# Kernel tuning notes

Measured on AMD Instinct MI355X. Metric: run time of the kernel, lower is better.

Reference implementation:

```python
import jax, jax.numpy as jnp
import numpy as np

N_HEADS = 8

def setup_inputs() -> dict:
    key = jax.random.key(0)
    ks = jax.random.split(key, 12)
    B, S2, C, H, W = 2, 2048, 1280, 256, 256
    s = 0.02  # weight init scale
    return {
        'hidden_states': jax.random.normal(ks[0], (B, S2, C), dtype=jnp.float32),
        'src_mask': (jax.random.uniform(ks[1], (B, 1, H, W)) > 0.5).astype(jnp.float32),
        'attn_wq': jax.random.normal(ks[2], (C, C), dtype=jnp.float32) * s,
        'attn_wk': jax.random.normal(ks[3], (C, C), dtype=jnp.float32) * s,
        'attn_wv': jax.random.normal(ks[4], (C, C), dtype=jnp.float32) * s,
        'out_w': jax.random.normal(ks[5], (C, C), dtype=jnp.float32) * s,
        'out_b': jnp.zeros((C,), dtype=jnp.float32),
        'proc_wq': jax.random.normal(ks[6], (C, C), dtype=jnp.float32) * s,
        'proc_wk': jax.random.normal(ks[7], (C, C), dtype=jnp.float32) * s,
        'proc_wv': jax.random.normal(ks[8], (C, C), dtype=jnp.float32) * s,
        'ww': jax.random.normal(ks[9], (C + 1, 1), dtype=jnp.float32) * s,
        'wb': jnp.zeros((1,), dtype=jnp.float32),
    }


def reference(hidden_states, src_mask, attn_wq, attn_wk, attn_wv, out_w, out_b,
              proc_wq, proc_wk, proc_wv, ww, wb):
    B, S2, C = hidden_states.shape
    S = S2 // 2  # condition_flag=False: sequence is two images concatenated
    _, _, H, W = src_mask.shape
    r = int(np.sqrt((H * W) / S))  # nearest-neighbor downsample ratio
    # F.interpolate(mode='nearest') with exact integer ratio == strided slice
    m = src_mask[:, 0, ::r, ::r].reshape(B, S, 1)          # [B, S, 1]
    mask = jnp.concatenate([m, m], axis=1)                 # [B, 2S, 1]
    # sigmoid gate blending the two query projections
    gate_in = jnp.concatenate([hidden_states, mask], axis=-1)  # [B, 2S, C+1]
    w = jax.nn.sigmoid(gate_in @ ww + wb)                  # [B, 2S, 1]
    query = (hidden_states @ attn_wq) * w + (hidden_states @ proc_wq) * (1.0 - w)
    # keys/values: first half through attn's projections, second half through processor's
    e1, e2 = hidden_states[:, :S], hidden_states[:, S:]
    key = jnp.concatenate([e1 @ attn_wk, e2 @ proc_wk], axis=1)
    value = jnp.concatenate([e1 @ attn_wv, e2 @ proc_wv], axis=1)
    d = C // N_HEADS
    def split_heads(x):
        return x.reshape(B, S2, N_HEADS, d).transpose(0, 2, 1, 3)  # [B, H, S2, d]
    qh, kh, vh = split_heads(query), split_heads(key), split_heads(value)
    scale = float(1.0 / np.sqrt(d))
    scores = jnp.einsum('bhqd,bhkd->bhqk', qh, kh) * scale
    probs = jax.nn.softmax(scores, axis=-1)
    out = jnp.einsum('bhqk,bhkd->bhqd', probs, vh)
    out = out.transpose(0, 2, 1, 3).reshape(B, S2, C)
    out = out @ out_w + out_b
    # residual connection, rescale_output_factor == 1
    return out + hidden_states
```

## Files before the change

kernel.cpp:

```cpp
#include <hip/hip_runtime.h>

typedef unsigned short u16;
typedef u16 u16x4 __attribute__((ext_vector_type(4)));
typedef u16 u16x8 __attribute__((ext_vector_type(8)));
typedef __bf16 bf16x8 __attribute__((ext_vector_type(8)));
typedef float f32x4 __attribute__((ext_vector_type(4)));
typedef unsigned u32x4 __attribute__((ext_vector_type(4)));

#define DEVI __device__ __forceinline__

#if __has_builtin(__builtin_amdgcn_exp2f)
#define EXP2F __builtin_amdgcn_exp2f
#else
#define EXP2F exp2f
#endif

DEVI u16 f2b(float f) {
  unsigned u = __builtin_bit_cast(unsigned, f);
  u += 0x7fffu + ((u >> 16) & 1u);
  return (u16)(u >> 16);
}

DEVI float b2f(u16 v) { return __builtin_bit_cast(float, (unsigned)v << 16); }

DEVI unsigned cvtpk_bf16(float lo, float hi) {
  unsigned r;
  asm("v_cvt_pk_bf16_f32 %0, %1, %2" : "=v"(r) : "v"(lo), "v"(hi));
  return r;
}

DEVI f32x4 mfma16(u16x8 a, u16x8 b, f32x4 c) {
  return __builtin_amdgcn_mfma_f32_16x16x32_bf16(
      __builtin_bit_cast(bf16x8, a), __builtin_bit_cast(bf16x8, b), c, 0, 0, 0);
}

DEVI void async_copy16(const u16* g, u16* l) {
  __builtin_amdgcn_global_load_lds(
      (__attribute__((address_space(1))) unsigned int*)(g),
      (__attribute__((address_space(3))) unsigned int*)(l), 16, 0, 0);
}

DEVI void fence_barrier() {
  asm volatile("" ::: "memory");
  __builtin_amdgcn_s_barrier();
  asm volatile("" ::: "memory");
}

__global__ void prep_kernel(const float* __restrict__ hs, const float* __restrict__ mask,
                            const float* __restrict__ ww, const float* __restrict__ wb,
                            u16* __restrict__ hsb, float* __restrict__ wgate) {
  int token = blockIdx.x;
  int tid = threadIdx.x;
  const float* row = hs + (size_t)token * 1280;
  u16* orow = hsb + (size_t)token * 1280;
  float acc = 0.f;
#pragma unroll
  for (int i = 0; i < 5; i++) {
    int c = i * 256 + tid;
    float v = row[c];
    orow[c] = f2b(v);
    acc += v * ww[c];
  }
#pragma unroll
  for (int off = 1; off < 64; off <<= 1) acc += __shfl_xor(acc, off);
  __shared__ float partial[4];
  int wid = tid >> 6;
  if ((tid & 63) == 0) partial[wid] = acc;
  __syncthreads();
  if (tid == 0) {
    float tot = partial[0] + partial[1] + partial[2] + partial[3];
    int b = token >> 11, t = token & 2047;
    int s = t & 1023;
    float mv = mask[b * 65536 + ((s >> 5) * 8) * 256 + (s & 31) * 8];
    float z = tot + mv * ww[1280] + wb[0];
    wgate[token] = 1.f / (1.f + __expf(-z));
  }
}

__global__ void wtrans_kernel(const float* w0, const float* w1, const float* w2,
                              const float* w3, const float* w4, const float* w5,
                              const float* w6, u16* __restrict__ out) {
  const float* src;
  switch (blockIdx.z) {
    case 0: src = w0; break; case 1: src = w1; break; case 2: src = w2; break;
    case 3: src = w3; break; case 4: src = w4; break; case 5: src = w5; break;
    default: src = w6; break;
  }
  u16* dst = out + (size_t)blockIdx.z * 1280 * 1280;
  __shared__ float tile[32][33];
  int tx = threadIdx.x & 31, ty = threadIdx.x >> 5;
  int k0 = blockIdx.x * 32, n0 = blockIdx.y * 32;
#pragma unroll
  for (int r = 0; r < 4; r++)
    tile[ty + r * 8][tx] = src[(size_t)(k0 + ty + r * 8) * 1280 + n0 + tx];
  __syncthreads();
#pragma unroll
  for (int r = 0; r < 4; r++)
    dst[(size_t)(n0 + ty + r * 8) * 1280 + k0 + tx] = f2b(tile[tx][ty + r * 8]);
}

__launch_bounds__(256)
__global__ void gemm_qkv_kernel(const u16* __restrict__ A, const u16* __restrict__ Wt,
                                u16* __restrict__ Qa, u16* __restrict__ Qp,
                                u16* __restrict__ Kout, u16* __restrict__ VTout) {
  const int K = 1280, N = 1280;
  const size_t WSZ = (size_t)1280 * 1280;
  __shared__ u16 As[128 * 32];
  __shared__ u16 Bs[128 * 32];

  int tid = threadIdx.x;
  int wid = tid >> 6, lane = tid & 63;
  int nb = blockIdx.x, mb = blockIdx.y, z = blockIdx.z;
  int m0 = mb * 128, n0 = nb * 128;
  bool first = ((m0 & 2047) < 1024);

  const u16* B;
  switch (z) {
    case 0:  B = Wt + 0 * WSZ; break;
    case 1:  B = Wt + 4 * WSZ; break;
    case 2:  B = first ? Wt + 1 * WSZ : Wt + 5 * WSZ; break;
    default: B = first ? Wt + 2 * WSZ : Wt + 6 * WSZ; break;
  }

  f32x4 zero = {0.f, 0.f, 0.f, 0.f};
  f32x4 acc[4][4];
#pragma unroll
  for (int i = 0; i < 4; i++)
#pragma unroll
    for (int j = 0; j < 4; j++) acc[i][j] = zero;

  int wr = wid >> 1, wc = wid & 1;

  for (int kk = 0; kk < 40; kk++) {
    int k0 = kk * 32;
#pragma unroll
    for (int i = 0; i < 2; i++) {
      int slot = i * 256 + tid;
      int row = slot >> 2, seg = slot & 3;
      async_copy16(A + (size_t)(m0 + row) * K + k0 + seg * 8, As + (size_t)(i * 256 + wid * 64) * 8);
      async_copy16(B + (size_t)(n0 + row) * K + k0 + seg * 8, Bs + (size_t)(i * 256 + wid * 64) * 8);
    }
    asm volatile("s_waitcnt vmcnt(0)" ::: "memory");
    __syncthreads();

    u16x8 af[4], bfr[4];
#pragma unroll
    for (int mi = 0; mi < 4; mi++)
      af[mi] = *(const u16x8*)(As + (wr * 64 + mi * 16 + (lane & 15)) * 32 + (lane >> 4) * 8);
#pragma unroll
    for (int ni = 0; ni < 4; ni++)
      bfr[ni] = *(const u16x8*)(Bs + (wc * 64 + ni * 16 + (lane & 15)) * 32 + (lane >> 4) * 8);
#pragma unroll
    for (int mi = 0; mi < 4; mi++)
#pragma unroll
      for (int ni = 0; ni < 4; ni++)
        acc[mi][ni] = mfma16(af[mi], bfr[ni], acc[mi][ni]);
    __syncthreads();
  }

  if (z == 3) {
#pragma unroll
    for (int mi = 0; mi < 4; mi++)
#pragma unroll
      for (int ni = 0; ni < 4; ni++) {
        int row0 = m0 + wr * 64 + mi * 16 + ((lane >> 4) << 2);
        int col = n0 + wc * 64 + ni * 16 + (lane & 15);
        int b = row0 >> 11, s = row0 & 2047;
        int h = col / 160, c_in = col - h * 160;
        u16x4 v = {f2b(acc[mi][ni][0]), f2b(acc[mi][ni][1]),
                   f2b(acc[mi][ni][2]), f2b(acc[mi][ni][3])};
        *(u16x4*)(VTout + ((size_t)(b * 8 + h) * 160 + c_in) * 2048 + s) = v;
      }
  } else {
    u16* Cb = (z == 0) ? Qa : (z == 1) ? Qp : Kout;
#pragma unroll
    for (int mi = 0; mi < 4; mi++)
#pragma unroll
      for (int ni = 0; ni < 4; ni++)
#pragma unroll
        for (int r = 0; r < 4; r++) {
          int row = m0 + wr * 64 + mi * 16 + ((lane >> 4) << 2) + r;
          int col = n0 + wc * 64 + ni * 16 + (lane & 15);
          Cb[(size_t)row * N + col] = f2b(acc[mi][ni][r]);
        }
  }
}

__global__ void qblend_kernel(u16* __restrict__ Qa, const u16* __restrict__ Qp,
                              const float* __restrict__ wgate, float qscale) {
  int idx = blockIdx.x * 256 + threadIdx.x;
  int token = idx / 160;
  float w = wgate[token];
  u16x8 qa = *(const u16x8*)(Qa + (size_t)idx * 8);
  u16x8 qp = *(const u16x8*)(Qp + (size_t)idx * 8);
  u16x8 o;
#pragma unroll
  for (int j = 0; j < 8; j++)
    o[j] = f2b((w * b2f(qa[j]) + (1.f - w) * b2f(qp[j])) * qscale);
  *(u16x8*)(Qa + (size_t)idx * 8) = o;
}

template <int SPLIT>
__launch_bounds__(256)
__global__ void flash_kernel(const u16* __restrict__ Q, const u16* __restrict__ Kg,
                             const u16* __restrict__ VTg, u16* __restrict__ O,
                             u16* __restrict__ Opart, float* __restrict__ MLbuf) {
  const int C = 1280;
  int bid = blockIdx.x;
  int qb = bid & 31, h = (bid >> 5) & 7, b = bid >> 8;
  int sp = (SPLIT > 1) ? (int)blockIdx.y : 0;
  int tid = threadIdx.x, wid = tid >> 6, lane = tid & 63;

  int t0, NT;
  if (SPLIT == 3) { t0 = sp * 11; NT = (sp < 2) ? 11 : 10; }
  else if (SPLIT == 1) { t0 = 0; NT = 32; }
  else { t0 = sp * (32 / SPLIT); NT = 32 / SPLIT; }

  const size_t baseQ = ((size_t)(b * 2048 + qb * 64)) * C + h * 160;
  const size_t baseK = ((size_t)(b * 2048)) * C + h * 160;
  const size_t baseVT = (size_t)(b * 8 + h) * 160 * 2048;

  __shared__ u16 Ks[64 * 168];
  __shared__ u16 Vts[160 * 64];

  const u16* kbase = Kg + baseK + (size_t)(t0 * 64) * C;
  const u16* vbase = VTg + baseVT + t0 * 64;
  unsigned koff[6];
#pragma unroll
  for (int j = 0; j < 6; j++) {
    int i = wid + 4 * j;
    if (i > 20) i = wid + 16;
    int gc = i * 64 + lane;
    int r = gc / 21, ch = gc - r * 21;
    int chs = ch < 20 ? ch : 19;
    koff[j] = (unsigned)(r * C + chs * 8);
  }
  unsigned voff[5];
#pragma unroll
  for (int j = 0; j < 5; j++) {
    int i = wid + 4 * j;
    int gc = i * 64 + lane;
    int c = gc >> 3, jj = gc & 7;
    voff[j] = (unsigned)(c * 2048 + ((jj ^ (c & 7)) << 3));
  }

#define STAGE_K()                                       \
  do {                                                  \
    _Pragma("unroll") for (int j = 0; j < 6; j++) {     \
      int i = wid + 4 * j;                              \
      if (i > 20) i = wid + 16;                         \
      async_copy16(kbase + koff[j], Ks + i * 512);      \
    }                                                   \
  } while (0)
#define STAGE_V()                                               \
  do {                                                          \
    _Pragma("unroll") for (int j = 0; j < 5; j++)               \
        async_copy16(vbase + voff[j], Vts + (wid + 4 * j) * 512); \
  } while (0)

  const int addr0 = ((lane & 15) + 16 * (((lane >> 4) * 2 + 0) & 3)) << 2;
  const int addr1 = ((lane & 15) + 16 * (((lane >> 4) * 2 + 1) & 3)) << 2;
  const bool hihalf = (lane >= 32);

  u16x8 qf[5];
  {
    int row = wid * 16 + (lane & 15);
    const u16* qrow = Q + baseQ + (size_t)row * C;
#pragma unroll
    for (int ks = 0; ks < 5; ks++)
      qf[ks] = *(const u16x8*)(qrow + ks * 32 + (lane >> 4) * 8);
  }

  f32x4 zero = {0.f, 0.f, 0.f, 0.f};
  f32x4 oacc[10];
#pragma unroll
  for (int i = 0; i < 10; i++) oacc[i] = zero;
  float mrow = -1e30f, lrow = 0.f;

  STAGE_K();
  STAGE_V();

  for (int kti = 0; kti < NT; kti++) {
    bool last = (kti == NT - 1);
    asm volatile("s_waitcnt vmcnt(5)" ::: "memory");
    fence_barrier();

    f32x4 sc[4];
#pragma unroll
    for (int ct = 0; ct < 4; ct++) {
      f32x4 a = zero;
#pragma unroll
      for (int ks = 0; ks < 5; ks++) {
        u16x8 kf = *(const u16x8*)(&Ks[(ct * 16 + (lane & 15)) * 168 + ks * 32 + (lane >> 4) * 8]);
        a = mfma16(kf, qf[ks], a);
      }
      sc[ct] = a;
    }

    fence_barrier();
    if (!last) { kbase += 64 * C; STAGE_K(); }

    float m = sc[0][0];
#pragma unroll
    for (int ct = 0; ct < 4; ct++)
#pragma unroll
      for (int r = 0; r < 4; r++) m = fmaxf(m, sc[ct][r]);
    m = fmaxf(m, __shfl_xor(m, 16));
    m = fmaxf(m, __shfl_xor(m, 32));

    if (__any(m > mrow + 8.f)) {
      float mnew = fmaxf(mrow, m);
      float alpha = EXP2F(mrow - mnew);
      mrow = mnew;
      float rs = 0.f;
#pragma unroll
      for (int ct = 0; ct < 4; ct++)
#pragma unroll
        for (int r = 0; r < 4; r++) {
          float p = EXP2F(sc[ct][r] - mnew);
          sc[ct][r] = p;
          rs += p;
        }
      lrow = lrow * alpha + rs;
#pragma unroll
      for (int ci = 0; ci < 10; ci++) oacc[ci] *= alpha;
    } else {
      float rs = 0.f;
#pragma unroll
      for (int ct = 0; ct < 4; ct++)
#pragma unroll
        for (int r = 0; r < 4; r++) {
          float p = EXP2F(sc[ct][r] - mrow);
          sc[ct][r] = p;
          rs += p;
        }
      lrow += rs;
    }

    unsigned pk0[4], pk1[4];
#pragma unroll
    for (int ct = 0; ct < 4; ct++) {
      pk0[ct] = cvtpk_bf16(sc[ct][0], sc[ct][1]);
      pk1[ct] = cvtpk_bf16(sc[ct][2], sc[ct][3]);
    }

    if (!last) { asm volatile("s_waitcnt vmcnt(6)" ::: "memory"); }
    else       { asm volatile("s_waitcnt vmcnt(0)" ::: "memory"); }
    fence_barrier();

#pragma unroll
    for (int kt2 = 0; kt2 < 2; kt2++) {
      const int cA = kt2 * 2, cB = kt2 * 2 + 1;
      int a0 = __builtin_amdgcn_ds_bpermute(addr0, (int)pk0[cA]);
      int a1 = __builtin_amdgcn_ds_bpermute(addr0, (int)pk1[cA]);
      int a2 = __builtin_amdgcn_ds_bpermute(addr1, (int)pk0[cA]);
      int a3 = __builtin_amdgcn_ds_bpermute(addr1, (int)pk1[cA]);
      int b0 = __builtin_amdgcn_ds_bpermute(addr0, (int)pk0[cB]);
      int b1 = __builtin_amdgcn_ds_bpermute(addr0, (int)pk1[cB]);
      int b2 = __builtin_amdgcn_ds_bpermute(addr1, (int)pk0[cB]);
      int b3 = __builtin_amdgcn_ds_bpermute(addr1, (int)pk1[cB]);
      u32x4 d;
      d[0] = (unsigned)(hihalf ? b0 : a0);
      d[1] = (unsigned)(hihalf ? b1 : a1);
      d[2] = (unsigned)(hihalf ? b2 : a2);
      d[3] = (unsigned)(hihalf ? b3 : a3);
      u16x8 pf = __builtin_bit_cast(u16x8, d);
#pragma unroll
      for (int ci = 0; ci < 10; ci++) {
        int c = ci * 16 + (lane & 15);
        int jl = kt2 * 4 + (lane >> 4);
        u16x8 vf = *(const u16x8*)(&Vts[c * 64 + ((jl ^ (c & 7)) << 3)]);
        oacc[ci] = mfma16(vf, pf, oacc[ci]);
      }
    }

    fence_barrier();
    if (!last) { vbase += 64; STAGE_V(); }
  }
#undef STAGE_K
#undef STAGE_V

  lrow += __shfl_xor(lrow, 16);
  lrow += __shfl_xor(lrow, 32);
  float linv = 1.f / lrow;

  int qrow = qb * 64 + wid * 16 + (lane & 15);
  if constexpr (SPLIT > 1) {
    size_t g0 = (size_t)sp * 4096 + (size_t)b * 2048 + qrow;
#pragma unroll
    for (int ci = 0; ci < 10; ci++) {
      int col = h * 160 + ci * 16 + ((lane >> 4) << 2);
      u16x4 v = {f2b(oacc[ci][0] * linv), f2b(oacc[ci][1] * linv),
                 f2b(oacc[ci][2] * linv), f2b(oacc[ci][3] * linv)};
      *(u16x4*)(Opart + g0 * 1280 + col) = v;
    }
    if (lane < 16) {
      size_t mi = (g0 * 8 + h) * 2;
      MLbuf[mi] = mrow;
      MLbuf[mi + 1] = lrow;
    }
  } else {
#pragma unroll
    for (int ci = 0; ci < 10; ci++) {
      int col = h * 160 + ci * 16 + ((lane >> 4) << 2);
      u16x4 v = {f2b(oacc[ci][0] * linv), f2b(oacc[ci][1] * linv),
                 f2b(oacc[ci][2] * linv), f2b(oacc[ci][3] * linv)};
      *(u16x4*)(O + ((size_t)(b * 2048) + qrow) * C + col) = v;
    }
  }
}

__global__ void combine_kernel(const u16* __restrict__ Opart, const float* __restrict__ MLbuf,
                               u16* __restrict__ O) {
  int idx = blockIdx.x * 256 + threadIdx.x;
  int token = idx / 160;
  int h = (idx - token * 160) / 20;
  size_t i0 = ((size_t)token * 8 + h) * 2;
  const size_t MLP = (size_t)4096 * 16;
  float m0 = MLbuf[i0], l0 = MLbuf[i0 + 1];
  float m1 = MLbuf[i0 + MLP], l1 = MLbuf[i0 + MLP + 1];
  float m2 = MLbuf[i0 + 2 * MLP], l2 = MLbuf[i0 + 2 * MLP + 1];
  float m = fmaxf(fmaxf(m0, m1), m2);
  float w0 = EXP2F(m0 - m) * l0, w1 = EXP2F(m1 - m) * l1, w2 = EXP2F(m2 - m) * l2;
  float inv = 1.f / (w0 + w1 + w2);
  w0 *= inv; w1 *= inv; w2 *= inv;
  const size_t OPP = (size_t)655360;
  u16x8 a = *(const u16x8*)(Opart + (size_t)idx * 8);
  u16x8 c = *(const u16x8*)(Opart + (OPP + idx) * 8);
  u16x8 d = *(const u16x8*)(Opart + (2 * OPP + idx) * 8);
  u16x8 o;
#pragma unroll
  for (int j = 0; j < 8; j++)
    o[j] = f2b(b2f(a[j]) * w0 + b2f(c[j]) * w1 + b2f(d[j]) * w2);
  *(u16x8*)(O + (size_t)idx * 8) = o;
}

__launch_bounds__(256)
__global__ void gemm_out_kernel(const u16* __restrict__ A, const u16* __restrict__ Bt,
                                float* __restrict__ Cf, const float* __restrict__ bias,
                                const float* __restrict__ resid) {
  const int K = 1280, N = 1280;
  __shared__ u16 As[128 * 32];
  __shared__ u16 Bs[128 * 32];

  int tid = threadIdx.x;
  int wid = tid >> 6, lane = tid & 63;
  int nb = blockIdx.x, mb = blockIdx.y;
  int m0 = mb * 128, n0 = nb * 128;

  f32x4 zero = {0.f, 0.f, 0.f, 0.f};
  f32x4 acc[4][4];
#pragma unroll
  for (int i = 0; i < 4; i++)
#pragma unroll
    for (int j = 0; j < 4; j++) acc[i][j] = zero;

  int wr = wid >> 1, wc = wid & 1;

  for (int kk = 0; kk < 40; kk++) {
    int k0 = kk * 32;
#pragma unroll
    for (int i = 0; i < 2; i++) {
      int slot = i * 256 + tid;
      int row = slot >> 2, seg = slot & 3;
      async_copy16(A + (size_t)(m0 + row) * K + k0 + seg * 8, As + (size_t)(i * 256 + wid * 64) * 8);
      async_copy16(Bt + (size_t)(n0 + row) * K + k0 + seg * 8, Bs + (size_t)(i * 256 + wid * 64) * 8);
    }
    asm volatile("s_waitcnt vmcnt(0)" ::: "memory");
    __syncthreads();

    u16x8 af[4], bfr[4];
#pragma unroll
    for (int mi = 0; mi < 4; mi++)
      af[mi] = *(const u16x8*)(As + (wr * 64 + mi * 16 + (lane & 15)) * 32 + (lane >> 4) * 8);
#pragma unroll
    for (int ni = 0; ni < 4; ni++)
      bfr[ni] = *(const u16x8*)(Bs + (wc * 64 + ni * 16 + (lane & 15)) * 32 + (lane >> 4) * 8);
#pragma unroll
    for (int mi = 0; mi < 4; mi++)
#pragma unroll
      for (int ni = 0; ni < 4; ni++)
        acc[mi][ni] = mfma16(af[mi], bfr[ni], acc[mi][ni]);
    __syncthreads();
  }

#pragma unroll
  for (int mi = 0; mi < 4; mi++)
#pragma unroll
    for (int ni = 0; ni < 4; ni++)
#pragma unroll
      for (int r = 0; r < 4; r++) {
        int row = m0 + wr * 64 + mi * 16 + ((lane >> 4) << 2) + r;
        int col = n0 + wc * 64 + ni * 16 + (lane & 15);
        Cf[(size_t)row * N + col] = acc[mi][ni][r] + bias[col] + resid[(size_t)row * N + col];
      }
}

extern "C" void kernel_launch(void* const* d_in, const int* in_sizes, int n_in,
                              void* d_out, int out_size, void* d_ws, size_t ws_size,
                              hipStream_t stream) {
  const float* hs      = (const float*)d_in[0];
  const float* mask    = (const float*)d_in[1];
  const float* attn_wq = (const float*)d_in[2];
  const float* attn_wk = (const float*)d_in[3];
  const float* attn_wv = (const float*)d_in[4];
  const float* out_w   = (const float*)d_in[5];
  const float* out_b   = (const float*)d_in[6];
  const float* proc_wq = (const float*)d_in[7];
  const float* proc_wk = (const float*)d_in[8];
  const float* proc_wv = (const float*)d_in[9];
  const float* ww      = (const float*)d_in[10];
  const float* wb      = (const float*)d_in[11];
  float* out = (float*)d_out;

  char* ws = (char*)d_ws;
  const size_t TOK = (size_t)4096 * 1280;
  u16* hsb = (u16*)(ws);
  u16* Qb  = (u16*)(ws + 2 * TOK);
  u16* Kb  = (u16*)(ws + 4 * TOK);
  u16* VTb = (u16*)(ws + 6 * TOK);
  u16* AOb = (u16*)(ws + 8 * TOK);
  u16* Wt  = (u16*)(ws + 10 * TOK);
  float* wgate = (float*)(ws + 10 * TOK + (size_t)7 * 1280 * 1280 * 2);
  char* extra = ws + 10 * TOK + (size_t)7 * 1280 * 1280 * 2 + 16384;
  u16* Opart = (u16*)extra;
  float* MLbuf = (float*)(extra + (size_t)3 * 4096 * 1280 * 2);
  size_t need = (size_t)(extra - ws) + (size_t)3 * 4096 * 1280 * 2 + (size_t)3 * 4096 * 8 * 8;

  prep_kernel<<<4096, 256, 0, stream>>>(hs, mask, ww, wb, hsb, wgate);
  wtrans_kernel<<<dim3(40, 40, 7), 256, 0, stream>>>(attn_wq, attn_wk, attn_wv, out_w,
                                                     proc_wq, proc_wk, proc_wv, Wt);
  const size_t WSZ = (size_t)1280 * 1280;
  gemm_qkv_kernel<<<dim3(10, 32, 4), 256, 0, stream>>>(hsb, Wt, Qb, AOb, Kb, VTb);
  const float qscale = 0.11405505533858971f;
  qblend_kernel<<<2560, 256, 0, stream>>>(Qb, AOb, wgate, qscale);

  if (ws_size >= need) {
    flash_kernel<3><<<dim3(512, 3), 256, 0, stream>>>(Qb, Kb, VTb, nullptr, Opart, MLbuf);
    combine_kernel<<<2560, 256, 0, stream>>>(Opart, MLbuf, AOb);
  } else {
    flash_kernel<1><<<dim3(512, 1), 256, 0, stream>>>(Qb, Kb, VTb, AOb, nullptr, nullptr);
  }
  gemm_out_kernel<<<dim3(10, 32), 256, 0, stream>>>(AOb, Wt + 3 * WSZ, out, out_b, hs);
}
```

Measured before the change: 240.4 us.

## Fuse query gate blend into QKV GEMM epilogue and swizzle flash K tile

The QKV GEMM now computes both query projections in the same block for z<2, with each block taking 64 output columns from each weight. The sigmoid-gated blend and scale are applied in the epilogue, which removes the separate qblend kernel and its extra read/write pass over two query buffers. Separately, the flash kernel's K shared tile drops its 168-element padded rows in favour of an XOR swizzle. That cuts async copies per tile from 6 to 5 and shrinks LDS use. Inner loop shapes change for the dual case, which may affect register pressure and scheduling.

```diff
diff --git a/kernel.cpp b/kernel.cpp
--- a/kernel.cpp
+++ b/kernel.cpp
@@ -101,26 +101,27 @@
 
 __launch_bounds__(256)
 __global__ void gemm_qkv_kernel(const u16* __restrict__ A, const u16* __restrict__ Wt,
-                                u16* __restrict__ Qa, u16* __restrict__ Qp,
-                                u16* __restrict__ Kout, u16* __restrict__ VTout) {
+                                const float* __restrict__ wgate, float qscale,
+                                u16* __restrict__ Qout, u16* __restrict__ Kout,
+                                u16* __restrict__ VTout) {
   const int K = 1280, N = 1280;
   const size_t WSZ = (size_t)1280 * 1280;
   __shared__ u16 As[128 * 32];
-  __shared__ u16 Bs[128 * 32];
+  __shared__ u16 Bs[64 * 32];
+  __shared__ u16 Bs2[64 * 32];
 
   int tid = threadIdx.x;
   int wid = tid >> 6, lane = tid & 63;
+  int q = lane & 15, jl = lane >> 4;
   int nb = blockIdx.x, mb = blockIdx.y, z = blockIdx.z;
   int m0 = mb * 128, n0 = nb * 128;
+  bool dual = (z < 2);
   bool first = ((m0 & 2047) < 1024);
 
-  const u16* B;
-  switch (z) {
-    case 0:  B = Wt + 0 * WSZ; break;
-    case 1:  B = Wt + 4 * WSZ; break;
-    case 2:  B = first ? Wt + 1 * WSZ : Wt + 5 * WSZ; break;
-    default: B = first ? Wt + 2 * WSZ : Wt + 6 * WSZ; break;
-  }
+  const u16 *B0, *B1;
+  if (dual)        { B0 = Wt + 0 * WSZ; B1 = Wt + 4 * WSZ; }
+  else if (z == 2) { B0 = first ? Wt + 1 * WSZ : Wt + 5 * WSZ; B1 = B0; }
+  else             { B0 = first ? Wt + 2 * WSZ : Wt + 6 * WSZ; B1 = B0; }
 
   f32x4 zero = {0.f, 0.f, 0.f, 0.f};
   f32x4 acc[4][4];
@@ -130,6 +131,7 @@
     for (int j = 0; j < 4; j++) acc[i][j] = zero;
 
   int wr = wid >> 1, wc = wid & 1;
+  int brow = tid >> 2, bseg = tid & 3;
 
   for (int kk = 0; kk < 40; kk++) {
     int k0 = kk * 32;
@@ -138,66 +140,87 @@
       int slot = i * 256 + tid;
       int row = slot >> 2, seg = slot & 3;
       async_copy16(A + (size_t)(m0 + row) * K + k0 + seg * 8, As + (size_t)(i * 256 + wid * 64) * 8);
-      async_copy16(B + (size_t)(n0 + row) * K + k0 + seg * 8, Bs + (size_t)(i * 256 + wid * 64) * 8);
+    }
+    if (dual) {
+      int nrow = n0 + (z << 6) + brow;
+      async_copy16(B0 + (size_t)nrow * K + k0 + bseg * 8, Bs + (size_t)tid * 8);
+      async_copy16(B1 + (size_t)nrow * K + k0 + bseg * 8, Bs2 + (size_t)tid * 8);
+    } else {
+      async_copy16(B0 + (size_t)(n0 + brow) * K + k0 + bseg * 8, Bs + (size_t)tid * 8);
+      async_copy16(B0 + (size_t)(n0 + 64 + brow) * K + k0 + bseg * 8, Bs2 + (size_t)tid * 8);
     }
     asm volatile("s_waitcnt vmcnt(0)" ::: "memory");
     __syncthreads();
 
-    u16x8 af[4], bfr[4];
+    u16x8 af[4];
 #pragma unroll
     for (int mi = 0; mi < 4; mi++)
-      af[mi] = *(const u16x8*)(As + (wr * 64 + mi * 16 + (lane & 15)) * 32 + (lane >> 4) * 8);
-#pragma unroll
-    for (int ni = 0; ni < 4; ni++)
-      bfr[ni] = *(const u16x8*)(Bs + (wc * 64 + ni * 16 + (lane & 15)) * 32 + (lane >> 4) * 8);
+      af[mi] = *(const u16x8*)(As + (wr * 64 + mi * 16 + q) * 32 + jl * 8);
+    if (dual) {
+#pragma unroll
+      for (int ni = 0; ni < 2; ni++) {
+        u16x8 bf0 = *(const u16x8*)(Bs + (wc * 32 + ni * 16 + q) * 32 + jl * 8);
+        u16x8 bf1 = *(const u16x8*)(Bs2 + (wc * 32 + ni * 16 + q) * 32 + jl * 8);
+#pragma unroll
+        for (int mi = 0; mi < 4; mi++) {
+          acc[mi][ni] = mfma16(af[mi], bf0, acc[mi][ni]);
+          acc[mi][2 + ni] = mfma16(af[mi], bf1, acc[mi][2 + ni]);
+        }
+      }
+    } else {
+      const u16* Bsel = wc ? Bs2 : Bs;
+      u16x8 bfr[4];
+#pragma unroll
+      for (int ni = 0; ni < 4; ni++)
+        bfr[ni] = *(const u16x8*)(Bsel + (ni * 16 + q) * 32 + jl * 8);
+#pragma unroll
+      for (int mi = 0; mi < 4; mi++)
+#pragma unroll
+        for (int ni = 0; ni < 4; ni++)
+          acc[mi][ni] = mfma16(af[mi], bfr[ni], acc[mi][ni]);
+    }
+    __syncthreads();
+  }
+
+  if (dual) {
 #pragma unroll
     for (int mi = 0; mi < 4; mi++)
 #pragma unroll
+      for (int r = 0; r < 4; r++) {
+        int row = m0 + wr * 64 + mi * 16 + (jl << 2) + r;
+        float w = wgate[row];
+#pragma unroll
+        for (int ni = 0; ni < 2; ni++) {
+          int col = n0 + (z << 6) + wc * 32 + ni * 16 + q;
+          float v = (w * acc[mi][ni][r] + (1.f - w) * acc[mi][2 + ni][r]) * qscale;
+          Qout[(size_t)row * N + col] = f2b(v);
+        }
+      }
+  } else if (z == 2) {
+#pragma unroll
+    for (int mi = 0; mi < 4; mi++)
+#pragma unroll
       for (int ni = 0; ni < 4; ni++)
-        acc[mi][ni] = mfma16(af[mi], bfr[ni], acc[mi][ni]);
-    __syncthreads();
-  }
-
-  if (z == 3) {
+#pragma unroll
+        for (int r = 0; r < 4; r++) {
+          int row = m0 + wr * 64 + mi * 16 + (jl << 2) + r;
+          int col = n0 + wc * 64 + ni * 16 + q;
+          Kout[(size_t)row * N + col] = f2b(acc[mi][ni][r]);
+        }
+  } else {
 #pragma unroll
     for (int mi = 0; mi < 4; mi++)
 #pragma unroll
       for (int ni = 0; ni < 4; ni++) {
-        int row0 = m0 + wr * 64 + mi * 16 + ((lane >> 4) << 2);
-        int col = n0 + wc * 64 + ni * 16 + (lane & 15);
+        int row0 = m0 + wr * 64 + mi * 16 + (jl << 2);
+        int col = n0 + wc * 64 + ni * 16 + q;
         int b = row0 >> 11, s = row0 & 2047;
         int h = col / 160, c_in = col - h * 160;
         u16x4 v = {f2b(acc[mi][ni][0]), f2b(acc[mi][ni][1]),
                    f2b(acc[mi][ni][2]), f2b(acc[mi][ni][3])};
         *(u16x4*)(VTout + ((size_t)(b * 8 + h) * 160 + c_in) * 2048 + s) = v;
       }
-  } else {
-    u16* Cb = (z == 0) ? Qa : (z == 1) ? Qp : Kout;
-#pragma unroll
-    for (int mi = 0; mi < 4; mi++)
-#pragma unroll
-      for (int ni = 0; ni < 4; ni++)
-#pragma unroll
-        for (int r = 0; r < 4; r++) {
-          int row = m0 + wr * 64 + mi * 16 + ((lane >> 4) << 2) + r;
-          int col = n0 + wc * 64 + ni * 16 + (lane & 15);
-          Cb[(size_t)row * N + col] = f2b(acc[mi][ni][r]);
-        }
-  }
-}
-
-__global__ void qblend_kernel(u16* __restrict__ Qa, const u16* __restrict__ Qp,
-                              const float* __restrict__ wgate, float qscale) {
-  int idx = blockIdx.x * 256 + threadIdx.x;
-  int token = idx / 160;
-  float w = wgate[token];
-  u16x8 qa = *(const u16x8*)(Qa + (size_t)idx * 8);
-  u16x8 qp = *(const u16x8*)(Qp + (size_t)idx * 8);
-  u16x8 o;
-#pragma unroll
-  for (int j = 0; j < 8; j++)
-    o[j] = f2b((w * b2f(qa[j]) + (1.f - w) * b2f(qp[j])) * qscale);
-  *(u16x8*)(Qa + (size_t)idx * 8) = o;
+  }
 }
 
 template <int SPLIT>
@@ -210,6 +233,7 @@
   int qb = bid & 31, h = (bid >> 5) & 7, b = bid >> 8;
   int sp = (SPLIT > 1) ? (int)blockIdx.y : 0;
   int tid = threadIdx.x, wid = tid >> 6, lane = tid & 63;
+  int q = lane & 15, jl = lane >> 4;
 
   int t0, NT;
   if (SPLIT == 3) { t0 = sp * 11; NT = (sp < 2) ? 11 : 10; }
@@ -220,55 +244,50 @@
   const size_t baseK = ((size_t)(b * 2048)) * C + h * 160;
   const size_t baseVT = (size_t)(b * 8 + h) * 160 * 2048;
 
-  __shared__ u16 Ks[64 * 168];
+  __shared__ u16 Ks[64 * 160];
   __shared__ u16 Vts[160 * 64];
 
   const u16* kbase = Kg + baseK + (size_t)(t0 * 64) * C;
   const u16* vbase = VTg + baseVT + t0 * 64;
-  unsigned koff[6];
-#pragma unroll
-  for (int j = 0; j < 6; j++) {
-    int i = wid + 4 * j;
-    if (i > 20) i = wid + 16;
-    int gc = i * 64 + lane;
-    int r = gc / 21, ch = gc - r * 21;
-    int chs = ch < 20 ? ch : 19;
-    koff[j] = (unsigned)(r * C + chs * 8);
+  unsigned koff[5];
+#pragma unroll
+  for (int j = 0; j < 5; j++) {
+    int s = (wid + 4 * j) * 64 + lane;
+    int r = s / 20, cp = s - r * 20;
+    int c = cp ^ ((r >> 1) & 3);
+    koff[j] = (unsigned)(r * C + c * 8);
   }
   unsigned voff[5];
 #pragma unroll
   for (int j = 0; j < 5; j++) {
-    int i = wid + 4 * j;
-    int gc = i * 64 + lane;
+    int gc = (wid + 4 * j) * 64 + lane;
     int c = gc >> 3, jj = gc & 7;
     voff[j] = (unsigned)(c * 2048 + ((jj ^ (c & 7)) << 3));
   }
 
-#define STAGE_K()                                       \
-  do {                                                  \
-    _Pragma("unroll") for (int j = 0; j < 6; j++) {     \
-      int i = wid + 4 * j;                              \
-      if (i > 20) i = wid + 16;                         \
-      async_copy16(kbase + koff[j], Ks + i * 512);      \
-    }                                                   \
+#define STAGE_K()                                                  \
+  do {                                                             \
+    _Pragma("unroll") for (int j = 0; j < 5; j++)                  \
+        async_copy16(kbase + koff[j], Ks + (wid + 4 * j) * 512);   \
   } while (0)
-#define STAGE_V()                                               \
-  do {                                                          \
-    _Pragma("unroll") for (int j = 0; j < 5; j++)               \
-        async_copy16(vbase + voff[j], Vts + (wid + 4 * j) * 512); \
+#define STAGE_V()                                                  \
+  do {                                                             \
+    _Pragma("unroll") for (int j = 0; j < 5; j++)                  \
+        async_copy16(vbase + voff[j], Vts + (wid + 4 * j) * 512);  \
   } while (0)
 
-  const int addr0 = ((lane & 15) + 16 * (((lane >> 4) * 2 + 0) & 3)) << 2;
-  const int addr1 = ((lane & 15) + 16 * (((lane >> 4) * 2 + 1) & 3)) << 2;
+  const int kro = ((jl ^ ((q >> 1) & 3)) << 3);
+
+  const int addr0 = (q + 16 * ((jl * 2 + 0) & 3)) << 2;
+  const int addr1 = (q + 16 * ((jl * 2 + 1) & 3)) << 2;
   const bool hihalf = (lane >= 32);
 
   u16x8 qf[5];
   {
-    int row = wid * 16 + (lane & 15);
-    const u16* qrow = Q + baseQ + (size_t)row * C;
+    const u16* qrow = Q + baseQ + (size_t)(wid * 16 + q) * C;
 #pragma unroll
     for (int ks = 0; ks < 5; ks++)
-      qf[ks] = *(const u16x8*)(qrow + ks * 32 + (lane >> 4) * 8);
+      qf[ks] = *(const u16x8*)(qrow + ks * 32 + jl * 8);
   }
 
   f32x4 zero = {0.f, 0.f, 0.f, 0.f};
@@ -291,7 +310,7 @@
       f32x4 a = zero;
 #pragma unroll
       for (int ks = 0; ks < 5; ks++) {
-        u16x8 kf = *(const u16x8*)(&Ks[(ct * 16 + (lane & 15)) * 168 + ks * 32 + (lane >> 4) * 8]);
+        u16x8 kf = *(const u16x8*)(&Ks[(ct * 16 + q) * 160 + ks * 32 + kro]);
         a = mfma16(kf, qf[ks], a);
       }
       sc[ct] = a;
@@ -344,7 +363,7 @@
       pk1[ct] = cvtpk_bf16(sc[ct][2], sc[ct][3]);
     }
 
-    if (!last) { asm volatile("s_waitcnt vmcnt(6)" ::: "memory"); }
+    if (!last) { asm volatile("s_waitcnt vmcnt(5)" ::: "memory"); }
     else       { asm volatile("s_waitcnt vmcnt(0)" ::: "memory"); }
     fence_barrier();
 
@@ -367,9 +386,9 @@
       u16x8 pf = __builtin_bit_cast(u16x8, d);
 #pragma unroll
       for (int ci = 0; ci < 10; ci++) {
-        int c = ci * 16 + (lane & 15);
-        int jl = kt2 * 4 + (lane >> 4);
-        u16x8 vf = *(const u16x8*)(&Vts[c * 64 + ((jl ^ (c & 7)) << 3)]);
+        int c = ci * 16 + q;
+        int jj = kt2 * 4 + jl;
+        u16x8 vf = *(const u16x8*)(&Vts[c * 64 + ((jj ^ (c & 7)) << 3)]);
         oacc[ci] = mfma16(vf, pf, oacc[ci]);
       }
     }
@@ -384,12 +403,12 @@
   lrow += __shfl_xor(lrow, 32);
   float linv = 1.f / lrow;
 
-  int qrow = qb * 64 + wid * 16 + (lane & 15);
+  int qrow = qb * 64 + wid * 16 + q;
   if constexpr (SPLIT > 1) {
     size_t g0 = (size_t)sp * 4096 + (size_t)b * 2048 + qrow;
 #pragma unroll
     for (int ci = 0; ci < 10; ci++) {
-      int col = h * 160 + ci * 16 + ((lane >> 4) << 2);
+      int col = h * 160 + ci * 16 + (jl << 2);
       u16x4 v = {f2b(oacc[ci][0] * linv), f2b(oacc[ci][1] * linv),
                  f2b(oacc[ci][2] * linv), f2b(oacc[ci][3] * linv)};
       *(u16x4*)(Opart + g0 * 1280 + col) = v;
@@ -402,7 +421,7 @@
   } else {
 #pragma unroll
     for (int ci = 0; ci < 10; ci++) {
-      int col = h * 160 + ci * 16 + ((lane >> 4) << 2);
+      int col = h * 160 + ci * 16 + (jl << 2);
       u16x4 v = {f2b(oacc[ci][0] * linv), f2b(oacc[ci][1] * linv),
                  f2b(oacc[ci][2] * linv), f2b(oacc[ci][3] * linv)};
       *(u16x4*)(O + ((size_t)(b * 2048) + qrow) * C + col) = v;
@@ -531,9 +550,8 @@
   wtrans_kernel<<<dim3(40, 40, 7), 256, 0, stream>>>(attn_wq, attn_wk, attn_wv, out_w,
                                                      proc_wq, proc_wk, proc_wv, Wt);
   const size_t WSZ = (size_t)1280 * 1280;
-  gemm_qkv_kernel<<<dim3(10, 32, 4), 256, 0, stream>>>(hsb, Wt, Qb, AOb, Kb, VTb);
   const float qscale = 0.11405505533858971f;
-  qblend_kernel<<<2560, 256, 0, stream>>>(Qb, AOb, wgate, qscale);
+  gemm_qkv_kernel<<<dim3(10, 32, 4), 256, 0, stream>>>(hsb, Wt, wgate, qscale, Qb, Kb, VTb);
 
   if (ws_size >= need) {
     flash_kernel<3><<<dim3(512, 3), 256, 0, stream>>>(Qb, Kb, VTb, nullptr, Opart, MLbuf);
```

New measurement: 322.6 us. 1.34x slower.
